# Kernel tuning notes

Measured on AMD Instinct MI355X. Metric: run time of the kernel, lower is better.

Reference implementation:

```python
import jax, jax.numpy as jnp
import numpy as np

T, B, IN, H = 256, 64, 2048, 1024
NUM_LAYERS = 3


def setup_inputs() -> dict:
    key = jax.random.key(0)
    ks = jax.random.split(key, 1 + 4 * NUM_LAYERS)
    s = 1.0 / np.sqrt(H)  # torch LSTM default init scale
    d = {
        "x": jax.random.normal(ks[0], (T, B, IN), dtype=jnp.float32),
        "h0": jnp.zeros((NUM_LAYERS, B, H), dtype=jnp.float32),
        "c0": jnp.zeros((NUM_LAYERS, B, H), dtype=jnp.float32),
    }
    for l in range(NUM_LAYERS):
        in_dim = IN if l == 0 else H
        k = ks[1 + 4 * l:5 + 4 * l]
        d[f"w_ih{l}"] = jax.random.uniform(k[0], (4 * H, in_dim), jnp.float32, -s, s)
        d[f"w_hh{l}"] = jax.random.uniform(k[1], (4 * H, H), jnp.float32, -s, s)
        d[f"b_ih{l}"] = jax.random.uniform(k[2], (4 * H,), jnp.float32, -s, s)
        d[f"b_hh{l}"] = jax.random.uniform(k[3], (4 * H,), jnp.float32, -s, s)
    return d


def _lstm_layer(x_seq, h0, c0, w_ih, w_hh, b_ih, b_hh):
    # Hoist the input projection out of the recurrence: [T,B,4H]
    xg = jnp.einsum('tbi,gi->tbg', x_seq, w_ih) + (b_ih + b_hh)
    w_hh_t = w_hh.T  # [H, 4H]

    def step(carry, xg_t):
        h, c = carry
        gates = xg_t + h @ w_hh_t  # [B, 4H]
        i, f, g, o = jnp.split(gates, 4, axis=-1)  # PyTorch gate order i,f,g,o
        i = jax.nn.sigmoid(i)
        f = jax.nn.sigmoid(f)
        g = jnp.tanh(g)
        o = jax.nn.sigmoid(o)
        c = f * c + i * g
        h = o * jnp.tanh(c)
        return (h, c), h

    (hT, cT), ys = jax.lax.scan(step, (h0, c0), xg)
    return ys, hT, cT


def reference(x, h0, c0,
              w_ih0, w_hh0, b_ih0, b_hh0,
              w_ih1, w_hh1, b_ih1, b_hh1,
              w_ih2, w_hh2, b_ih2, b_hh2):
    layers = [
        (w_ih0, w_hh0, b_ih0, b_hh0),
        (w_ih1, w_hh1, b_ih1, b_hh1),
        (w_ih2, w_hh2, b_ih2, b_hh2),
    ]
    y = x
    hs, cs = [], []
    for l, (wi, wh, bi, bh) in enumerate(layers):
        y, hT, cT = _lstm_layer(y, h0[l], c0[l], wi, wh, bi, bh)
        hs.append(hT)
        cs.append(cT)
    return y, (jnp.stack(hs), jnp.stack(cs))
```

## Files before the change

kernel.cpp:

```cpp
#include <hip/hip_runtime.h>

#define AS1 __attribute__((address_space(1)))
#define AS3 __attribute__((address_space(3)))

typedef unsigned short u16;
typedef unsigned long long u64;
typedef __attribute__((ext_vector_type(8))) unsigned short u16x8;
typedef __attribute__((ext_vector_type(8))) __bf16 bf16x8;
typedef __attribute__((ext_vector_type(4))) float f32x4;

#define TT 256
#define BB 64
#define IN_DIM 2048
#define HH 1024
#define GG 4096
#define MM 16384
#define NBLK 192

__device__ __forceinline__ u16 f2bf(float f) {
  unsigned u = __builtin_bit_cast(unsigned, f);
  return (u16)((u + 0x7fffu + ((u >> 16) & 1u)) >> 16);
}
__device__ __forceinline__ float bf2f(u16 h) {
  unsigned u = ((unsigned)h) << 16;
  return __builtin_bit_cast(float, u);
}
__device__ __forceinline__ f32x4 mfma16(u16x8 a, u16x8 b, f32x4 c) {
  return __builtin_amdgcn_mfma_f32_16x16x32_bf16(
      __builtin_bit_cast(bf16x8, a), __builtin_bit_cast(bf16x8, b), c, 0, 0, 0);
}
__device__ __forceinline__ float sigmoid_fast(float x) {
  float e = __expf(-x);
  return __fdividef(1.f, 1.f + e);
}
__device__ __forceinline__ float tanh_fast(float x) {
  float xx = fmaxf(x, -30.f);
  float e = __expf(-2.f * xx);
  return __fdividef(1.f - e, 1.f + e);
}

__global__ void cvt_bf16_k(const float* __restrict__ in, u16* __restrict__ out, long n) {
  long i = ((long)blockIdx.x * blockDim.x + threadIdx.x) * 4;
  long stride = (long)gridDim.x * blockDim.x * 4;
  for (; i < n; i += stride) {
    float4 v = *(const float4*)(in + i);
    ushort4 o = { f2bf(v.x), f2bf(v.y), f2bf(v.z), f2bf(v.w) };
    *(ushort4*)(out + i) = o;
  }
}

__global__ void bias_sum_k(const float* __restrict__ a, const float* __restrict__ b,
                           float* __restrict__ o, int n) {
  int i = blockIdx.x * blockDim.x + threadIdx.x;
  if (i < n) o[i] = a[i] + b[i];
}

__global__ __launch_bounds__(256) void gemm_bt_bias(
    const u16* __restrict__ A, const u16* __restrict__ W,
    const float* __restrict__ bias, u16* __restrict__ C, int K) {
  __shared__ u16 As[128 * 32];
  __shared__ u16 Bs[128 * 32];
  const int tid = threadIdx.x, wave = tid >> 6, lane = tid & 63;
  const size_t m0 = (size_t)blockIdx.x * 128, n0 = (size_t)blockIdx.y * 128;
  const int wm = (wave >> 1) * 64, wn = (wave & 1) * 64;
  const int lr = lane & 15, lq = lane >> 4;
  const int srow = wave * 16 + (lane >> 2);
  const int scol = (lane & 3) * 8;
  const u16* Ap = A + (m0 + srow) * K + scol;
  const u16* Wp = W + (n0 + srow) * K + scol;
  u16* AsB0 = &As[(wave * 64) * 8];
  u16* AsB1 = &As[(256 + wave * 64) * 8];
  u16* BsB0 = &Bs[(wave * 64) * 8];
  u16* BsB1 = &Bs[(256 + wave * 64) * 8];

  f32x4 acc[4][4];
#pragma unroll
  for (int i = 0; i < 4; ++i)
#pragma unroll
    for (int j = 0; j < 4; ++j) acc[i][j] = (f32x4){0.f, 0.f, 0.f, 0.f};

  for (int k0 = 0; k0 < K; k0 += 32) {
    __builtin_amdgcn_global_load_lds((AS1 const void*)(Ap + k0), (AS3 void*)AsB0, 16, 0, 0);
    __builtin_amdgcn_global_load_lds((AS1 const void*)(Ap + (size_t)64 * K + k0), (AS3 void*)AsB1, 16, 0, 0);
    __builtin_amdgcn_global_load_lds((AS1 const void*)(Wp + k0), (AS3 void*)BsB0, 16, 0, 0);
    __builtin_amdgcn_global_load_lds((AS1 const void*)(Wp + (size_t)64 * K + k0), (AS3 void*)BsB1, 16, 0, 0);
    __syncthreads();
    u16x8 af[4], bfr[4];
#pragma unroll
    for (int i = 0; i < 4; ++i) af[i] = *(const u16x8*)&As[(wm + i * 16 + lr) * 32 + lq * 8];
#pragma unroll
    for (int j = 0; j < 4; ++j) bfr[j] = *(const u16x8*)&Bs[(wn + j * 16 + lr) * 32 + lq * 8];
#pragma unroll
    for (int i = 0; i < 4; ++i)
#pragma unroll
      for (int j = 0; j < 4; ++j) acc[i][j] = mfma16(af[i], bfr[j], acc[i][j]);
    __syncthreads();
  }
#pragma unroll
  for (int i = 0; i < 4; ++i) {
#pragma unroll
    for (int j = 0; j < 4; ++j) {
      int n = (int)n0 + wn + j * 16 + lr;
      float bv = bias[n];
      size_t coff = (size_t)((n & 1023) * 4 + (n >> 10));
#pragma unroll
      for (int r = 0; r < 4; ++r) {
        int m = wm + i * 16 + lq * 4 + r;
        C[(m0 + m) * GG + coff] = f2bf(acc[i][j][r] + bv);
      }
    }
  }
}

__device__ __forceinline__ void gbar(unsigned* bar) {
  __builtin_amdgcn_s_waitcnt(0);
  __syncthreads();
  if (threadIdx.x == 0) {
    unsigned g = __hip_atomic_load(&bar[1], __ATOMIC_RELAXED, __HIP_MEMORY_SCOPE_AGENT);
    unsigned a = __hip_atomic_fetch_add(&bar[0], 1u, __ATOMIC_RELAXED, __HIP_MEMORY_SCOPE_AGENT);
    if (a == NBLK - 1) {
      __hip_atomic_store(&bar[0], 0u, __ATOMIC_RELAXED, __HIP_MEMORY_SCOPE_AGENT);
      __hip_atomic_store(&bar[1], g + 1u, __ATOMIC_RELAXED, __HIP_MEMORY_SCOPE_AGENT);
    } else {
      int spins = 0;
      while (__hip_atomic_load(&bar[1], __ATOMIC_RELAXED, __HIP_MEMORY_SCOPE_AGENT) == g) {
        __builtin_amdgcn_s_sleep(2);
        if ((++spins & 63) == 0)
          (void)__hip_atomic_load(&bar[1], __ATOMIC_ACQUIRE, __HIP_MEMORY_SCOPE_AGENT);
      }
    }
  }
  __syncthreads();
  __builtin_amdgcn_fence(__ATOMIC_ACQUIRE, "agent");
}

__global__ __launch_bounds__(256, 1) void lstm_pipe(
    const u16* __restrict__ whh0, const u16* __restrict__ whh1, const u16* __restrict__ whh2,
    const u16* __restrict__ wih1, const u16* __restrict__ wih2,
    const u16* __restrict__ xgi,
    const float* __restrict__ bias,
    const float* __restrict__ h0,
    const float* __restrict__ c0,
    u16* __restrict__ hbuf,
    float* __restrict__ yout,
    float* __restrict__ hTo, float* __restrict__ cTo,
    unsigned* __restrict__ bar) {
  __shared__ float pbuf[4][64][68];
  const int tid = threadIdx.x, wave = tid >> 6, lane = tid & 63;
  const int layer = blockIdx.x >> 6;
  const int j0 = (blockIdx.x & 63) * 16;
  const int lr = lane & 15, lq = lane >> 4;
  const int kbase = wave * 256;
  const u16* Wh = layer == 0 ? whh0 : (layer == 1 ? whh1 : whh2);
  const u16* Wx = layer == 2 ? wih2 : wih1;

  u16x8 breg_h[4][8], breg_x[4][8];
#pragma unroll
  for (int g = 0; g < 4; ++g) {
    const u16* wrow = Wh + (size_t)(g * 1024 + j0 + lr) * 1024 + kbase + lq * 8;
#pragma unroll
    for (int ks = 0; ks < 8; ++ks) breg_h[g][ks] = *(const u16x8*)(wrow + ks * 32);
  }
  if (layer > 0) {
#pragma unroll
    for (int g = 0; g < 4; ++g) {
      const u16* wrow = Wx + (size_t)(g * 1024 + j0 + lr) * 1024 + kbase + lq * 8;
#pragma unroll
      for (int ks = 0; ks < 8; ++ks) breg_x[g][ks] = *(const u16x8*)(wrow + ks * 32);
    }
  }

  const int m = tid >> 2, jc = (tid & 3) * 4;
  float creg[4], bias_r[4][4];
#pragma unroll
  for (int d = 0; d < 4; ++d)
    creg[d] = c0[(size_t)layer * 65536 + (size_t)m * 1024 + j0 + jc + d];
  if (layer > 0) {
#pragma unroll
    for (int g = 0; g < 4; ++g)
#pragma unroll
      for (int d = 0; d < 4; ++d)
        bias_r[g][d] = bias[(size_t)layer * GG + g * 1024 + j0 + jc + d];
  }
  {
    u64 hp = 0;
#pragma unroll
    for (int d = 0; d < 4; ++d)
      hp |= (u64)f2bf(h0[(size_t)layer * 65536 + (size_t)m * 1024 + j0 + jc + d]) << (16 * d);
    __hip_atomic_store((u64*)(hbuf + (size_t)(layer * 2 + 1) * 65536 + (size_t)m * 1024 + j0 + jc),
                       hp, __ATOMIC_RELAXED, __HIP_MEMORY_SCOPE_AGENT);
  }
  gbar(bar);

  for (int s = 0; s < TT + 2; ++s) {
    const int t = s - layer;
    if (t >= 0 && t < TT) {
      f32x4 acc[4][4];
#pragma unroll
      for (int i = 0; i < 4; ++i)
#pragma unroll
        for (int g = 0; g < 4; ++g) acc[i][g] = (f32x4){0.f, 0.f, 0.f, 0.f};

      const u16* hprev = hbuf + (size_t)(layer * 2 + ((t + 1) & 1)) * 65536;
#pragma unroll
      for (int ks = 0; ks < 8; ++ks) {
        u16x8 ao[4];
#pragma unroll
        for (int i = 0; i < 4; ++i)
          ao[i] = *(const u16x8*)(hprev + (size_t)(i * 16 + lr) * 1024 + kbase + ks * 32 + lq * 8);
#pragma unroll
        for (int g = 0; g < 4; ++g)
#pragma unroll
          for (int i = 0; i < 4; ++i) acc[i][g] = mfma16(ao[i], breg_h[g][ks], acc[i][g]);
      }
      if (layer > 0) {
        const u16* hbel = hbuf + (size_t)((layer - 1) * 2 + (t & 1)) * 65536;
#pragma unroll
        for (int ks = 0; ks < 8; ++ks) {
          u16x8 ab[4];
#pragma unroll
          for (int i = 0; i < 4; ++i)
            ab[i] = *(const u16x8*)(hbel + (size_t)(i * 16 + lr) * 1024 + kbase + ks * 32 + lq * 8);
#pragma unroll
          for (int g = 0; g < 4; ++g)
#pragma unroll
            for (int i = 0; i < 4; ++i) acc[i][g] = mfma16(ab[i], breg_x[g][ks], acc[i][g]);
        }
      }
#pragma unroll
      for (int i = 0; i < 4; ++i)
#pragma unroll
        for (int g = 0; g < 4; ++g)
          *(f32x4*)&pbuf[wave][g * 16 + lr][i * 16 + lq * 4] = acc[i][g];
      __syncthreads();

      float pre[4][4];
#pragma unroll
      for (int g = 0; g < 4; ++g)
#pragma unroll
        for (int d = 0; d < 4; ++d)
          pre[d][g] = pbuf[0][g * 16 + jc + d][m] + pbuf[1][g * 16 + jc + d][m] +
                      pbuf[2][g * 16 + jc + d][m] + pbuf[3][g * 16 + jc + d][m];
      if (layer == 0) {
        const u16* xr = xgi + ((size_t)(t * BB + m)) * GG + (size_t)(j0 + jc) * 4;
        u16x8 xa = *(const u16x8*)xr;
        u16x8 xb = *(const u16x8*)(xr + 8);
#pragma unroll
        for (int d = 0; d < 2; ++d)
#pragma unroll
          for (int g = 0; g < 4; ++g) {
            pre[d][g] += bf2f(xa[d * 4 + g]);
            pre[d + 2][g] += bf2f(xb[d * 4 + g]);
          }
      } else {
#pragma unroll
        for (int d = 0; d < 4; ++d)
#pragma unroll
          for (int g = 0; g < 4; ++g) pre[d][g] += bias_r[g][d];
      }
      float hv[4];
#pragma unroll
      for (int d = 0; d < 4; ++d) {
        float ii = sigmoid_fast(pre[d][0]);
        float ff = sigmoid_fast(pre[d][1]);
        float gg = tanh_fast(pre[d][2]);
        float oo = sigmoid_fast(pre[d][3]);
        float c = ff * creg[d] + ii * gg;
        creg[d] = c;
        hv[d] = oo * tanh_fast(c);
      }
      u64 hp = ((u64)f2bf(hv[0])) | ((u64)f2bf(hv[1]) << 16) |
               ((u64)f2bf(hv[2]) << 32) | ((u64)f2bf(hv[3]) << 48);
      __hip_atomic_store((u64*)(hbuf + (size_t)(layer * 2 + (t & 1)) * 65536 + (size_t)m * 1024 + j0 + jc),
                         hp, __ATOMIC_RELAXED, __HIP_MEMORY_SCOPE_AGENT);
      if (layer == 2) {
        float4 yv = { hv[0], hv[1], hv[2], hv[3] };
        *(float4*)(yout + ((size_t)(t * BB + m)) * 1024 + j0 + jc) = yv;
      }
      if (t == TT - 1) {
        float4 hvv = { hv[0], hv[1], hv[2], hv[3] };
        float4 cvv = { creg[0], creg[1], creg[2], creg[3] };
        *(float4*)(hTo + (size_t)layer * 65536 + (size_t)m * 1024 + j0 + jc) = hvv;
        *(float4*)(cTo + (size_t)layer * 65536 + (size_t)m * 1024 + j0 + jc) = cvv;
      }
    }
    if (s != TT + 1) gbar(bar);
  }
}

#define O_BAR   ((size_t)0)
#define O_BIAS  ((size_t)256)
#define O_HB    (O_BIAS + 49152)
#define O_XBF   (O_HB + 786432)
#define O_XGI   (O_XBF + 67108864)
#define O_WIH0  (O_XGI + 134217728)
#define O_WIH1  (O_WIH0 + 16777216)
#define O_WIH2  (O_WIH1 + 8388608)
#define O_WHH0  (O_WIH2 + 8388608)
#define O_WHH1  (O_WHH0 + 8388608)
#define O_WHH2  (O_WHH1 + 8388608)

extern "C" void kernel_launch(void* const* d_in, const int* in_sizes, int n_in,
                              void* d_out, int out_size, void* d_ws, size_t ws_size,
                              hipStream_t stream) {
  const float* x = (const float*)d_in[0];
  const float* h0 = (const float*)d_in[1];
  const float* c0 = (const float*)d_in[2];
  char* ws = (char*)d_ws;
  unsigned* bar = (unsigned*)(ws + O_BAR);
  float* bias = (float*)(ws + O_BIAS);
  u16* hbuf = (u16*)(ws + O_HB);
  u16* xbf = (u16*)(ws + O_XBF);
  u16* xgi = (u16*)(ws + O_XGI);
  u16* wih[3] = { (u16*)(ws + O_WIH0), (u16*)(ws + O_WIH1), (u16*)(ws + O_WIH2) };
  u16* whh[3] = { (u16*)(ws + O_WHH0), (u16*)(ws + O_WHH1), (u16*)(ws + O_WHH2) };
  float* youtf = (float*)d_out;
  float* hTo = (float*)d_out + (size_t)TT * BB * HH;
  float* cTo = hTo + 3 * BB * HH;

  hipMemsetAsync(bar, 0, 256, stream);
  cvt_bf16_k<<<4096, 256, 0, stream>>>(x, xbf, (long)MM * IN_DIM);
  for (int l = 0; l < 3; ++l) {
    long wn = (long)GG * (l == 0 ? IN_DIM : HH);
    cvt_bf16_k<<<2048, 256, 0, stream>>>((const float*)d_in[3 + 4 * l], wih[l], wn);
    cvt_bf16_k<<<2048, 256, 0, stream>>>((const float*)d_in[4 + 4 * l], whh[l], (long)GG * HH);
    bias_sum_k<<<16, 256, 0, stream>>>((const float*)d_in[5 + 4 * l],
                                       (const float*)d_in[6 + 4 * l], bias + l * GG, GG);
  }
  gemm_bt_bias<<<dim3(128, 32), 256, 0, stream>>>(xbf, wih[0], bias, xgi, IN_DIM);
  lstm_pipe<<<NBLK, 256, 0, stream>>>(whh[0], whh[1], whh[2], wih[1], wih[2],
                                      xgi, bias, h0, c0, hbuf, youtf, hTo, cTo, bar);
}
```

Before: 6.108 ms.

## Split gate columns across 8 waves and double-buffer h loads in LSTM pipe

Doubles the workgroup to 512 threads. Each of the 8 waves now handles two of the four gates for one quarter of K, which halves the per-wave weight registers and the MFMA chain length per time step. The activation loads are software-pipelined with two register buffers. The layer-0 xgi load is issued before the matmul, and the per-thread bias moves to LDS. The aim is to shorten the latency-bound per-step critical path and hide global load latency, at the cost of more threads per block and extra LDS use.

```diff
diff --git a/kernel.cpp b/kernel.cpp
--- a/kernel.cpp
+++ b/kernel.cpp
@@ -134,7 +134,7 @@
   __builtin_amdgcn_fence(__ATOMIC_ACQUIRE, "agent");
 }
 
-__global__ __launch_bounds__(256, 1) void lstm_pipe(
+__global__ __launch_bounds__(512, 2) void lstm_pipe(
     const u16* __restrict__ whh0, const u16* __restrict__ whh1, const u16* __restrict__ whh2,
     const u16* __restrict__ wih1, const u16* __restrict__ wih2,
     const u16* __restrict__ xgi,
@@ -146,121 +146,131 @@
     float* __restrict__ hTo, float* __restrict__ cTo,
     unsigned* __restrict__ bar) {
   __shared__ float pbuf[4][64][68];
+  __shared__ float sbias[512][9];
   const int tid = threadIdx.x, wave = tid >> 6, lane = tid & 63;
   const int layer = blockIdx.x >> 6;
   const int j0 = (blockIdx.x & 63) * 16;
   const int lr = lane & 15, lq = lane >> 4;
-  const int kbase = wave * 256;
+  const int gp = wave >> 2, kq = wave & 3;
+  const int kbase = kq * 256;
   const u16* Wh = layer == 0 ? whh0 : (layer == 1 ? whh1 : whh2);
   const u16* Wx = layer == 2 ? wih2 : wih1;
 
-  u16x8 breg_h[4][8], breg_x[4][8];
-#pragma unroll
-  for (int g = 0; g < 4; ++g) {
-    const u16* wrow = Wh + (size_t)(g * 1024 + j0 + lr) * 1024 + kbase + lq * 8;
-#pragma unroll
-    for (int ks = 0; ks < 8; ++ks) breg_h[g][ks] = *(const u16x8*)(wrow + ks * 32);
+  u16x8 breg_h[2][8], breg_x[2][8];
+#pragma unroll
+  for (int g2 = 0; g2 < 2; ++g2) {
+    const u16* wrow = Wh + (size_t)((gp * 2 + g2) * 1024 + j0 + lr) * 1024 + kbase + lq * 8;
+#pragma unroll
+    for (int ks = 0; ks < 8; ++ks) breg_h[g2][ks] = *(const u16x8*)(wrow + ks * 32);
   }
   if (layer > 0) {
 #pragma unroll
-    for (int g = 0; g < 4; ++g) {
-      const u16* wrow = Wx + (size_t)(g * 1024 + j0 + lr) * 1024 + kbase + lq * 8;
-#pragma unroll
-      for (int ks = 0; ks < 8; ++ks) breg_x[g][ks] = *(const u16x8*)(wrow + ks * 32);
+    for (int g2 = 0; g2 < 2; ++g2) {
+      const u16* wrow = Wx + (size_t)((gp * 2 + g2) * 1024 + j0 + lr) * 1024 + kbase + lq * 8;
+#pragma unroll
+      for (int ks = 0; ks < 8; ++ks) breg_x[g2][ks] = *(const u16x8*)(wrow + ks * 32);
     }
   }
 
-  const int m = tid >> 2, jc = (tid & 3) * 4;
-  float creg[4], bias_r[4][4];
-#pragma unroll
-  for (int d = 0; d < 4; ++d)
+  const int m = tid >> 3, jc = (tid & 7) * 2;
+  float creg[2];
+#pragma unroll
+  for (int d = 0; d < 2; ++d)
     creg[d] = c0[(size_t)layer * 65536 + (size_t)m * 1024 + j0 + jc + d];
   if (layer > 0) {
 #pragma unroll
     for (int g = 0; g < 4; ++g)
 #pragma unroll
-      for (int d = 0; d < 4; ++d)
-        bias_r[g][d] = bias[(size_t)layer * GG + g * 1024 + j0 + jc + d];
+      for (int d = 0; d < 2; ++d)
+        sbias[tid][g * 2 + d] = bias[(size_t)layer * GG + g * 1024 + j0 + jc + d];
   }
   {
-    u64 hp = 0;
-#pragma unroll
-    for (int d = 0; d < 4; ++d)
-      hp |= (u64)f2bf(h0[(size_t)layer * 65536 + (size_t)m * 1024 + j0 + jc + d]) << (16 * d);
-    __hip_atomic_store((u64*)(hbuf + (size_t)(layer * 2 + 1) * 65536 + (size_t)m * 1024 + j0 + jc),
+    unsigned hp = (unsigned)f2bf(h0[(size_t)layer * 65536 + (size_t)m * 1024 + j0 + jc]) |
+                  ((unsigned)f2bf(h0[(size_t)layer * 65536 + (size_t)m * 1024 + j0 + jc + 1]) << 16);
+    __hip_atomic_store((unsigned*)(hbuf + (size_t)(layer * 2 + 1) * 65536 + (size_t)m * 1024 + j0 + jc),
                        hp, __ATOMIC_RELAXED, __HIP_MEMORY_SCOPE_AGENT);
   }
   gbar(bar);
+
+#define LDH(dst, kk) do { _Pragma("unroll") \
+  for (int i = 0; i < 4; ++i) \
+    dst[i] = *(const u16x8*)(hprev + (size_t)(i * 16 + lr) * 1024 + kbase + (kk) * 32 + lq * 8); \
+  } while (0)
+#define LDX(dst, kk) do { _Pragma("unroll") \
+  for (int i = 0; i < 4; ++i) \
+    dst[i] = *(const u16x8*)(hbel + (size_t)(i * 16 + lr) * 1024 + kbase + (kk) * 32 + lq * 8); \
+  } while (0)
+#define FMH(src, kk) do { _Pragma("unroll") \
+  for (int g2 = 0; g2 < 2; ++g2) { _Pragma("unroll") \
+    for (int i = 0; i < 4; ++i) acc[i][g2] = mfma16(src[i], breg_h[g2][kk], acc[i][g2]); } \
+  } while (0)
+#define FMX(src, kk) do { _Pragma("unroll") \
+  for (int g2 = 0; g2 < 2; ++g2) { _Pragma("unroll") \
+    for (int i = 0; i < 4; ++i) acc[i][g2] = mfma16(src[i], breg_x[g2][kk], acc[i][g2]); } \
+  } while (0)
 
   for (int s = 0; s < TT + 2; ++s) {
     const int t = s - layer;
     if (t >= 0 && t < TT) {
-      f32x4 acc[4][4];
+      f32x4 acc[4][2];
 #pragma unroll
       for (int i = 0; i < 4; ++i)
 #pragma unroll
-        for (int g = 0; g < 4; ++g) acc[i][g] = (f32x4){0.f, 0.f, 0.f, 0.f};
+        for (int g2 = 0; g2 < 2; ++g2) acc[i][g2] = (f32x4){0.f, 0.f, 0.f, 0.f};
 
       const u16* hprev = hbuf + (size_t)(layer * 2 + ((t + 1) & 1)) * 65536;
-#pragma unroll
-      for (int ks = 0; ks < 8; ++ks) {
-        u16x8 ao[4];
-#pragma unroll
-        for (int i = 0; i < 4; ++i)
-          ao[i] = *(const u16x8*)(hprev + (size_t)(i * 16 + lr) * 1024 + kbase + ks * 32 + lq * 8);
-#pragma unroll
-        for (int g = 0; g < 4; ++g)
-#pragma unroll
-          for (int i = 0; i < 4; ++i) acc[i][g] = mfma16(ao[i], breg_h[g][ks], acc[i][g]);
-      }
-      if (layer > 0) {
+      u16x8 xv = {};
+      if (layer == 0) {
+        xv = *(const u16x8*)(xgi + ((size_t)(t * BB + m)) * GG + (size_t)(j0 + jc) * 4);
+        u16x8 a0[4], a1[4];
+        LDH(a0, 0);
+#pragma unroll
+        for (int ks = 0; ks < 8; ks += 2) {
+          if (ks + 1 < 8) LDH(a1, ks + 1);
+          FMH(a0, ks);
+          if (ks + 2 < 8) LDH(a0, ks + 2);
+          if (ks + 1 < 8) FMH(a1, ks + 1);
+        }
+      } else {
         const u16* hbel = hbuf + (size_t)((layer - 1) * 2 + (t & 1)) * 65536;
-#pragma unroll
-        for (int ks = 0; ks < 8; ++ks) {
-          u16x8 ab[4];
-#pragma unroll
-          for (int i = 0; i < 4; ++i)
-            ab[i] = *(const u16x8*)(hbel + (size_t)(i * 16 + lr) * 1024 + kbase + ks * 32 + lq * 8);
-#pragma unroll
-          for (int g = 0; g < 4; ++g)
-#pragma unroll
-            for (int i = 0; i < 4; ++i) acc[i][g] = mfma16(ab[i], breg_x[g][ks], acc[i][g]);
+        u16x8 a0[4], b0[4], a1[4], b1[4];
+        LDH(a0, 0); LDX(b0, 0);
+#pragma unroll
+        for (int ks = 0; ks < 8; ks += 2) {
+          if (ks + 1 < 8) { LDH(a1, ks + 1); LDX(b1, ks + 1); }
+          FMH(a0, ks); FMX(b0, ks);
+          if (ks + 2 < 8) { LDH(a0, ks + 2); LDX(b0, ks + 2); }
+          if (ks + 1 < 8) { FMH(a1, ks + 1); FMX(b1, ks + 1); }
         }
       }
 #pragma unroll
       for (int i = 0; i < 4; ++i)
 #pragma unroll
-        for (int g = 0; g < 4; ++g)
-          *(f32x4*)&pbuf[wave][g * 16 + lr][i * 16 + lq * 4] = acc[i][g];
+        for (int g2 = 0; g2 < 2; ++g2)
+          *(f32x4*)&pbuf[kq][(gp * 2 + g2) * 16 + lr][i * 16 + lq * 4] = acc[i][g2];
       __syncthreads();
 
-      float pre[4][4];
+      float pre[2][4];
 #pragma unroll
       for (int g = 0; g < 4; ++g)
 #pragma unroll
-        for (int d = 0; d < 4; ++d)
+        for (int d = 0; d < 2; ++d)
           pre[d][g] = pbuf[0][g * 16 + jc + d][m] + pbuf[1][g * 16 + jc + d][m] +
                       pbuf[2][g * 16 + jc + d][m] + pbuf[3][g * 16 + jc + d][m];
       if (layer == 0) {
-        const u16* xr = xgi + ((size_t)(t * BB + m)) * GG + (size_t)(j0 + jc) * 4;
-        u16x8 xa = *(const u16x8*)xr;
-        u16x8 xb = *(const u16x8*)(xr + 8);
 #pragma unroll
         for (int d = 0; d < 2; ++d)
 #pragma unroll
-          for (int g = 0; g < 4; ++g) {
-            pre[d][g] += bf2f(xa[d * 4 + g]);
-            pre[d + 2][g] += bf2f(xb[d * 4 + g]);
-          }
+          for (int g = 0; g < 4; ++g) pre[d][g] += bf2f(xv[d * 4 + g]);
       } else {
 #pragma unroll
-        for (int d = 0; d < 4; ++d)
-#pragma unroll
-          for (int g = 0; g < 4; ++g) pre[d][g] += bias_r[g][d];
-      }
-      float hv[4];
-#pragma unroll
-      for (int d = 0; d < 4; ++d) {
+        for (int d = 0; d < 2; ++d)
+#pragma unroll
+          for (int g = 0; g < 4; ++g) pre[d][g] += sbias[tid][g * 2 + d];
+      }
+      float hv[2];
+#pragma unroll
+      for (int d = 0; d < 2; ++d) {
         float ii = sigmoid_fast(pre[d][0]);
         float ff = sigmoid_fast(pre[d][1]);
         float gg = tanh_fast(pre[d][2]);
@@ -269,23 +279,26 @@
         creg[d] = c;
         hv[d] = oo * tanh_fast(c);
       }
-      u64 hp = ((u64)f2bf(hv[0])) | ((u64)f2bf(hv[1]) << 16) |
-               ((u64)f2bf(hv[2]) << 32) | ((u64)f2bf(hv[3]) << 48);
-      __hip_atomic_store((u64*)(hbuf + (size_t)(layer * 2 + (t & 1)) * 65536 + (size_t)m * 1024 + j0 + jc),
+      unsigned hp = (unsigned)f2bf(hv[0]) | ((unsigned)f2bf(hv[1]) << 16);
+      __hip_atomic_store((unsigned*)(hbuf + (size_t)(layer * 2 + (t & 1)) * 65536 + (size_t)m * 1024 + j0 + jc),
                          hp, __ATOMIC_RELAXED, __HIP_MEMORY_SCOPE_AGENT);
       if (layer == 2) {
-        float4 yv = { hv[0], hv[1], hv[2], hv[3] };
-        *(float4*)(yout + ((size_t)(t * BB + m)) * 1024 + j0 + jc) = yv;
+        float2 yv = { hv[0], hv[1] };
+        *(float2*)(yout + ((size_t)(t * BB + m)) * 1024 + j0 + jc) = yv;
       }
       if (t == TT - 1) {
-        float4 hvv = { hv[0], hv[1], hv[2], hv[3] };
-        float4 cvv = { creg[0], creg[1], creg[2], creg[3] };
-        *(float4*)(hTo + (size_t)layer * 65536 + (size_t)m * 1024 + j0 + jc) = hvv;
-        *(float4*)(cTo + (size_t)layer * 65536 + (size_t)m * 1024 + j0 + jc) = cvv;
+        float2 hvv = { hv[0], hv[1] };
+        float2 cvv = { creg[0], creg[1] };
+        *(float2*)(hTo + (size_t)layer * 65536 + (size_t)m * 1024 + j0 + jc) = hvv;
+        *(float2*)(cTo + (size_t)layer * 65536 + (size_t)m * 1024 + j0 + jc) = cvv;
       }
     }
     if (s != TT + 1) gbar(bar);
   }
+#undef LDH
+#undef LDX
+#undef FMH
+#undef FMX
 }
 
 #define O_BAR   ((size_t)0)
@@ -328,6 +341,6 @@
                                        (const float*)d_in[6 + 4 * l], bias + l * GG, GG);
   }
   gemm_bt_bias<<<dim3(128, 32), 256, 0, stream>>>(xbf, wih[0], bias, xgi, IN_DIM);
-  lstm_pipe<<<NBLK, 256, 0, stream>>>(whh[0], whh[1], whh[2], wih[1], wih[2],
+  lstm_pipe<<<NBLK, 512, 0, stream>>>(whh[0], whh[1], whh[2], wih[1], wih[2],
                                       xgi, bias, h0, c0, hbuf, youtf, hTo, cTo, bar);
 }
```

Measured after the change: 9.175 ms. 1.5x slower.

## Split LSTM recurrence by gate across waves, stage W_hh in LDS

Applied to the files above, without the earlier changes.

Work in the recurrent kernel is now split so each wave owns one gate over the full K=1024, instead of all four gates over a quarter of K. The recurrent weights go into 128KB of LDS through global_load_lds, and the input weights for layers above 0 stay in registers. The cross-wave reduction through LDS becomes a plain gather, and h loads are software-pipelined with split accumulators. The cost is that each wave now reads the full h vector from global/L2 every step, and the kernel depends on LDS bandwidth and a large dynamic shared memory allocation.

```diff
diff --git a/kernel.cpp b/kernel.cpp
--- a/kernel.cpp
+++ b/kernel.cpp
@@ -16,6 +16,9 @@
 #define GG 4096
 #define MM 16384
 #define NBLK 192
+
+#define WLDS_BYTES 131072
+#define SMEM_BYTES (WLDS_BYTES + 4 * 16 * 68 * 4)
 
 __device__ __forceinline__ u16 f2bf(float f) {
   unsigned u = __builtin_bit_cast(unsigned, f);
@@ -145,29 +148,30 @@
     float* __restrict__ yout,
     float* __restrict__ hTo, float* __restrict__ cTo,
     unsigned* __restrict__ bar) {
-  __shared__ float pbuf[4][64][68];
+  extern __shared__ char smem[];
+  u16* wl = (u16*)smem;
+  float (*pbuf)[16][68] = (float(*)[16][68])(smem + WLDS_BYTES);
+
   const int tid = threadIdx.x, wave = tid >> 6, lane = tid & 63;
   const int layer = blockIdx.x >> 6;
   const int j0 = (blockIdx.x & 63) * 16;
   const int lr = lane & 15, lq = lane >> 4;
-  const int kbase = wave * 256;
   const u16* Wh = layer == 0 ? whh0 : (layer == 1 ? whh1 : whh2);
   const u16* Wx = layer == 2 ? wih2 : wih1;
 
-  u16x8 breg_h[4][8], breg_x[4][8];
-#pragma unroll
-  for (int g = 0; g < 4; ++g) {
-    const u16* wrow = Wh + (size_t)(g * 1024 + j0 + lr) * 1024 + kbase + lq * 8;
-#pragma unroll
-    for (int ks = 0; ks < 8; ++ks) breg_h[g][ks] = *(const u16x8*)(wrow + ks * 32);
-  }
+  {
+    const u16* src = Wh + (size_t)(wave * 1024 + j0 + lr) * 1024 + lq * 8;
+#pragma unroll
+    for (int ks = 0; ks < 32; ++ks)
+      __builtin_amdgcn_global_load_lds((AS1 const void*)(src + ks * 32),
+                                       (AS3 void*)(wl + (size_t)(wave * 32 + ks) * 512),
+                                       16, 0, 0);
+  }
+  u16x8 wx[32];
   if (layer > 0) {
-#pragma unroll
-    for (int g = 0; g < 4; ++g) {
-      const u16* wrow = Wx + (size_t)(g * 1024 + j0 + lr) * 1024 + kbase + lq * 8;
-#pragma unroll
-      for (int ks = 0; ks < 8; ++ks) breg_x[g][ks] = *(const u16x8*)(wrow + ks * 32);
-    }
+    const u16* src = Wx + (size_t)(wave * 1024 + j0 + lr) * 1024 + lq * 8;
+#pragma unroll
+    for (int ks = 0; ks < 32; ++ks) wx[ks] = *(const u16x8*)(src + ks * 32);
   }
 
   const int m = tid >> 2, jc = (tid & 3) * 4;
@@ -192,59 +196,80 @@
   }
   gbar(bar);
 
+#define WL(kk) (*(const u16x8*)(wl + ((size_t)(wave * 32 + (kk)) * 64 + lane) * 8))
+#define LDH(dst, kk) do { _Pragma("unroll") \
+  for (int i = 0; i < 4; ++i) \
+    dst[i] = *(const u16x8*)(hprev + (size_t)(i * 16 + lr) * 1024 + (kk) * 32 + lq * 8); \
+  } while (0)
+#define LDX(dst, kk) do { _Pragma("unroll") \
+  for (int i = 0; i < 4; ++i) \
+    dst[i] = *(const u16x8*)(hbel + (size_t)(i * 16 + lr) * 1024 + (kk) * 32 + lq * 8); \
+  } while (0)
+
   for (int s = 0; s < TT + 2; ++s) {
     const int t = s - layer;
     if (t >= 0 && t < TT) {
-      f32x4 acc[4][4];
-#pragma unroll
-      for (int i = 0; i < 4; ++i)
-#pragma unroll
-        for (int g = 0; g < 4; ++g) acc[i][g] = (f32x4){0.f, 0.f, 0.f, 0.f};
-
+      f32x4 acch[4], accx[4];
+#pragma unroll
+      for (int i = 0; i < 4; ++i) {
+        acch[i] = (f32x4){0.f, 0.f, 0.f, 0.f};
+        accx[i] = (f32x4){0.f, 0.f, 0.f, 0.f};
+      }
       const u16* hprev = hbuf + (size_t)(layer * 2 + ((t + 1) & 1)) * 65536;
-#pragma unroll
-      for (int ks = 0; ks < 8; ++ks) {
-        u16x8 ao[4];
-#pragma unroll
-        for (int i = 0; i < 4; ++i)
-          ao[i] = *(const u16x8*)(hprev + (size_t)(i * 16 + lr) * 1024 + kbase + ks * 32 + lq * 8);
-#pragma unroll
-        for (int g = 0; g < 4; ++g)
-#pragma unroll
-          for (int i = 0; i < 4; ++i) acc[i][g] = mfma16(ao[i], breg_h[g][ks], acc[i][g]);
-      }
-      if (layer > 0) {
-        const u16* hbel = hbuf + (size_t)((layer - 1) * 2 + (t & 1)) * 65536;
-#pragma unroll
-        for (int ks = 0; ks < 8; ++ks) {
-          u16x8 ab[4];
-#pragma unroll
-          for (int i = 0; i < 4; ++i)
-            ab[i] = *(const u16x8*)(hbel + (size_t)(i * 16 + lr) * 1024 + kbase + ks * 32 + lq * 8);
-#pragma unroll
-          for (int g = 0; g < 4; ++g)
-#pragma unroll
-            for (int i = 0; i < 4; ++i) acc[i][g] = mfma16(ab[i], breg_x[g][ks], acc[i][g]);
-        }
-      }
-#pragma unroll
-      for (int i = 0; i < 4; ++i)
-#pragma unroll
-        for (int g = 0; g < 4; ++g)
-          *(f32x4*)&pbuf[wave][g * 16 + lr][i * 16 + lq * 4] = acc[i][g];
-      __syncthreads();
-
-      float pre[4][4];
-#pragma unroll
-      for (int g = 0; g < 4; ++g)
-#pragma unroll
-        for (int d = 0; d < 4; ++d)
-          pre[d][g] = pbuf[0][g * 16 + jc + d][m] + pbuf[1][g * 16 + jc + d][m] +
-                      pbuf[2][g * 16 + jc + d][m] + pbuf[3][g * 16 + jc + d][m];
+      u16x8 xa = {}, xb = {};
       if (layer == 0) {
         const u16* xr = xgi + ((size_t)(t * BB + m)) * GG + (size_t)(j0 + jc) * 4;
-        u16x8 xa = *(const u16x8*)xr;
-        u16x8 xb = *(const u16x8*)(xr + 8);
+        xa = *(const u16x8*)xr;
+        xb = *(const u16x8*)(xr + 8);
+        u16x8 a0[4], a1[4];
+        LDH(a0, 0);
+#pragma unroll
+        for (int kk = 0; kk < 16; ++kk) {
+          const int ks = kk * 2;
+          LDH(a1, ks + 1);
+          u16x8 b0 = WL(ks);
+#pragma unroll
+          for (int i = 0; i < 4; ++i) acch[i] = mfma16(a0[i], b0, acch[i]);
+          if (kk < 15) LDH(a0, ks + 2);
+          u16x8 b1 = WL(ks + 1);
+#pragma unroll
+          for (int i = 0; i < 4; ++i) accx[i] = mfma16(a1[i], b1, accx[i]);
+        }
+      } else {
+        const u16* hbel = hbuf + (size_t)((layer - 1) * 2 + (t & 1)) * 65536;
+        u16x8 a0[4], b0v[4], a1[4], b1v[4];
+        LDH(a0, 0); LDX(b0v, 0);
+#pragma unroll
+        for (int kk = 0; kk < 16; ++kk) {
+          const int ks = kk * 2;
+          LDH(a1, ks + 1); LDX(b1v, ks + 1);
+          u16x8 bh0 = WL(ks);
+#pragma unroll
+          for (int i = 0; i < 4; ++i) acch[i] = mfma16(a0[i], bh0, acch[i]);
+#pragma unroll
+          for (int i = 0; i < 4; ++i) accx[i] = mfma16(b0v[i], wx[ks], accx[i]);
+          if (kk < 15) { LDH(a0, ks + 2); LDX(b0v, ks + 2); }
+          u16x8 bh1 = WL(ks + 1);
+#pragma unroll
+          for (int i = 0; i < 4; ++i) acch[i] = mfma16(a1[i], bh1, acch[i]);
+#pragma unroll
+          for (int i = 0; i < 4; ++i) accx[i] = mfma16(b1v[i], wx[ks + 1], accx[i]);
+        }
+      }
+#pragma unroll
+      for (int i = 0; i < 4; ++i) {
+        f32x4 sum = acch[i] + accx[i];
+        *(f32x4*)&pbuf[wave][lr][i * 16 + lq * 4] = sum;
+      }
+      __syncthreads();
+
+      float pre[4][4];
+#pragma unroll
+      for (int g = 0; g < 4; ++g)
+#pragma unroll
+        for (int d = 0; d < 4; ++d)
+          pre[d][g] = pbuf[g][jc + d][m];
+      if (layer == 0) {
 #pragma unroll
         for (int d = 0; d < 2; ++d)
 #pragma unroll
@@ -286,6 +311,9 @@
     }
     if (s != TT + 1) gbar(bar);
   }
+#undef WL
+#undef LDH
+#undef LDX
 }
 
 #define O_BAR   ((size_t)0)
@@ -318,6 +346,13 @@
   float* hTo = (float*)d_out + (size_t)TT * BB * HH;
   float* cTo = hTo + 3 * BB * HH;
 
+  static int smem_set = 0;
+  if (!smem_set) {
+    hipFuncSetAttribute((const void*)lstm_pipe,
+                        hipFuncAttributeMaxDynamicSharedMemorySize, SMEM_BYTES);
+    smem_set = 1;
+  }
+
   hipMemsetAsync(bar, 0, 256, stream);
   cvt_bf16_k<<<4096, 256, 0, stream>>>(x, xbf, (long)MM * IN_DIM);
   for (int l = 0; l < 3; ++l) {
@@ -328,6 +363,6 @@
                                        (const float*)d_in[6 + 4 * l], bias + l * GG, GG);
   }
   gemm_bt_bias<<<dim3(128, 32), 256, 0, stream>>>(xbf, wih[0], bias, xgi, IN_DIM);
-  lstm_pipe<<<NBLK, 256, 0, stream>>>(whh[0], whh[1], whh[2], wih[1], wih[2],
-                                      xgi, bias, h0, c0, hbuf, youtf, hTo, cTo, bar);
-}
+  lstm_pipe<<<NBLK, 256, SMEM_BYTES, stream>>>(whh[0], whh[1], whh[2], wih[1], wih[2],
+                                               xgi, bias, h0, c0, hbuf, youtf, hTo, cTo, bar);
+}
```

Measured after the change: 11.19 ms. +83.2%, slower.
